# Kernel tuning notes

Hardware: AMD Instinct MI355X
Metric: run time of the kernel (lower is better)

## Reference

```python
import jax, jax.numpy as jnp
import numpy as np

KR = 3  # kernel_range, SHIFT = 1


def _neighborhood(x):
    """x: [B,H,W,C] -> [B,H,W,9,C] stacking the 3x3 shifted views (zero pad),
    in the same (i,j) raster order as the original loop."""
    B, H, W, C = x.shape
    xp = jnp.pad(x, ((0, 0), (1, 1), (1, 1), (0, 0)))
    views = [xp[:, 1 + i:1 + i + H, 1 + j:1 + j + W, :]
             for i in (-1, 0, 1) for j in (-1, 0, 1)]
    return jnp.stack(views, axis=3)


def _conv(x, w, b):
    # tf.nn.conv2d NHWC, HWIO, SAME, stride 1
    return jax.lax.conv_general_dilated(
        x, w, window_strides=(1, 1), padding='SAME',
        dimension_numbers=('NHWC', 'HWIO', 'NHWC')) + b


def setup_inputs() -> dict:
    key = jax.random.key(0)
    ks = jax.random.split(key, 10)
    B, H, W, D = 8, 128, 128, 64
    g = lambda k, shape, fan: jax.random.normal(k, shape, jnp.float32) * np.float32(1.0 / np.sqrt(fan))
    return {
        'x': jax.random.normal(ks[0], (B, H, W, D), jnp.float32),
        'Q_P': g(ks[1], (D, D), D),
        'K_P': g(ks[2], (D, D), D),
        'V_P': g(ks[3], (D, D), D),
        'ff1_kernel': g(ks[4], (3, 3, D, D), 9 * D),
        'ff1_bias': jax.random.normal(ks[5], (D,), jnp.float32) * 0.01,
        'ff2_kernel': g(ks[6], (3, 3, D, 2 * D), 9 * D),
        'ff2_bias': jax.random.normal(ks[7], (2 * D,), jnp.float32) * 0.01,
        'ff3_kernel': g(ks[8], (3, 3, 2 * D, D), 9 * 2 * D),
        'ff3_bias': jax.random.normal(ks[9], (D,), jnp.float32) * 0.01,
    }


def reference(x, Q_P, K_P, V_P, ff1_kernel, ff1_bias, ff2_kernel, ff2_bias,
              ff3_kernel, ff3_bias):
    B, H, W, D = x.shape
    # 3x3 neighborhood gather (zero padded) and validity mask
    stk = _neighborhood(x)                                   # [B,H,W,9,D]
    mask = _neighborhood(jnp.ones((B, H, W, 1), x.dtype))    # [B,H,W,9,1]
    mask = mask[..., 0]                                      # [B,H,W,9]

    q = jnp.einsum('bhwd,de->bhwe', x, Q_P)                  # [B,H,W,D]
    k = jnp.einsum('bhwkd,de->bhwke', stk, K_P)              # [B,H,W,9,D]
    v = jnp.einsum('bhwkd,de->bhwke', stk, V_P)              # [B,H,W,9,D]

    # NOTE: faithful to original -- scores are MULTIPLIED by the mask
    # (masked entries become 0, not -inf) before softmax over the 9 neighbors.
    scores = jnp.einsum('bhwke,bhwe->bhwk', k, q) * mask     # [B,H,W,9]
    alpha = jax.nn.softmax(scores, axis=-1)
    attn = jnp.einsum('bhwk,bhwke->bhwe', alpha, v)          # [B,H,W,D]

    t = x + attn
    t_in = t
    t = jax.nn.relu(_conv(t, ff1_kernel, ff1_bias))
    t = jax.nn.relu(_conv(t, ff2_kernel, ff2_bias))
    t = jax.nn.relu(_conv(t, ff3_kernel, ff3_bias))
    return t_in + t
```

## Files before the change

kernel.cpp:

```cpp
#include <hip/hip_runtime.h>

typedef unsigned int uint32;
typedef unsigned short u16;
typedef short s16x8 __attribute__((ext_vector_type(8)));
typedef float f32x4 __attribute__((ext_vector_type(4)));

#define DEVINL static __device__ __forceinline__
#define MFMA16(a, b, c) __builtin_amdgcn_mfma_f32_16x16x32_bf16(a, b, c, 0, 0, 0)

DEVINL float bf2f(u16 u){ return __uint_as_float(((uint32)u) << 16); }
DEVINL u16 f2bf(float f){
  uint32 u = __float_as_uint(f);
  u += 0x7fffu + ((u >> 16) & 1u);
  return (u16)(u >> 16);
}
DEVINL uint32 pack2(float a, float b){
  return (uint32)f2bf(a) | (((uint32)f2bf(b)) << 16);
}

__global__ void detect_k(const uint32* __restrict__ x, uint32* __restrict__ flag){
  const int lane = threadIdx.x;
  int sane = 0;
  for (int i = 0; i < 32; ++i){
    uint32 u = x[i * 64 + lane];
    uint32 e = (u >> 7) & 0xffu;
    sane += (e >= 100u && e <= 150u) ? 1 : 0;
  }
  for (int off = 32; off >= 1; off >>= 1) sane += __shfl_xor(sane, off);
  if (lane == 0) *flag = (sane > 1024) ? 1u : 0u;
}

template<int M>
__global__ void cvtall_k(const void* s0, const void* s1, const void* s2,
                         const void* s3, const void* s4, const void* s5,
                         const void* s6, const void* s7, const void* s8,
                         float* __restrict__ wb, const uint32* __restrict__ flag)
{
  if (*flag != (uint32)M) return;
  const int i = blockIdx.x * 256 + threadIdx.x;
  if (i >= 196864) return;
  const void* s; int j;
  if      (i < 4096)   { s = s0; j = i; }
  else if (i < 8192)   { s = s1; j = i - 4096; }
  else if (i < 12288)  { s = s2; j = i - 8192; }
  else if (i < 49152)  { s = s3; j = i - 12288; }
  else if (i < 49216)  { s = s4; j = i - 49152; }
  else if (i < 122944) { s = s5; j = i - 49216; }
  else if (i < 123072) { s = s6; j = i - 122944; }
  else if (i < 196800) { s = s7; j = i - 123072; }
  else                 { s = s8; j = i - 196800; }
  wb[i] = M ? bf2f(((const u16*)s)[j]) : ((const float*)s)[j];
}

__global__ __launch_bounds__(256)
void xcvt_k(const void* __restrict__ x, u16* __restrict__ xb,
            const uint32* __restrict__ flag)
{
  if (*flag != 0u) return;
  const size_t i0 = ((size_t)blockIdx.x * 256 + threadIdx.x) * 8;
  const float4 f0 = ((const float4*)x)[i0 / 4];
  const float4 f1 = ((const float4*)x)[i0 / 4 + 1];
  uint4 o;
  o.x = pack2(f0.x, f0.y); o.y = pack2(f0.z, f0.w);
  o.z = pack2(f1.x, f1.y); o.w = pack2(f1.z, f1.w);
  *(uint4*)(xb + i0) = o;
}

__global__ void gcomp_k(const float* __restrict__ wb, u16* __restrict__ gt){
  const int t = blockIdx.x * 256 + threadIdx.x;
  const int d = t >> 6, c = t & 63;
  const float* __restrict__ K = wb + 4096;
  const float* __restrict__ Q = wb;
  float s = 0.f;
#pragma unroll
  for (int e = 0; e < 64; ++e) s = fmaf(K[d * 64 + e], Q[c * 64 + e], s);
  const u16 hi = f2bf(s);
  gt[t] = hi;
  gt[4096 + t] = f2bf(s - bf2f(hi));
}

__global__ void pack_k(const float* __restrict__ wb, u16* __restrict__ bb){
  int i = blockIdx.x * 256 + threadIdx.x;
  if (i < 4096){
    const int o = i >> 6, c = i & 63;
    bb[8192 + i] = f2bf(wb[8192 + c * 64 + o]);
    return;
  }
  i -= 4096;
  if (i < 36864){
    const int chunk = i >> 11, rr = i & 2047, co = rr >> 5, kkp = rr & 31;
    const int slot = (kkp >> 3) ^ ((co >> 1) & 3), kk = slot * 8 + (kkp & 7);
    const int tap = chunk >> 1, ci = (chunk & 1) * 32 + kk;
    bb[12288 + i] = f2bf(wb[12288 + (tap * 64 + ci) * 64 + co]);
    return;
  }
  i -= 36864;
  if (i < 73728){
    const int half = i / 36864, i2 = i - half * 36864;
    const int chunk = i2 >> 11, rr = i2 & 2047, co = rr >> 5, kkp = rr & 31;
    const int slot = (kkp >> 3) ^ ((co >> 1) & 3), kk = slot * 8 + (kkp & 7);
    const int tap = chunk >> 1, ci = (chunk & 1) * 32 + kk;
    bb[49152 + i] = f2bf(wb[49216 + (tap * 64 + ci) * 128 + half * 64 + co]);
    return;
  }
  i -= 73728;
  {
    const int chunk = i >> 11, rr = i & 2047, co = rr >> 5, kkp = rr & 31;
    const int slot = (kkp >> 3) ^ ((co >> 1) & 3), kk = slot * 8 + (kkp & 7);
    const int tap = chunk >> 2, ci = (chunk & 3) * 32 + kk;
    bb[122880 + i] = f2bf(wb[123072 + (tap * 128 + ci) * 64 + co]);
  }
}

template<int ROWS, int CIN, int STRIDE>
DEVINL void stage_tile(const u16* __restrict__ img_base, int h0, int w0, u16* lds){
  constexpr int CH8 = CIN / 8;
  constexpr int NCH = ROWS * 66 * CH8;
  for (int idx = threadIdx.x; idx < NCH; idx += 256){
    const int row  = idx / (66 * CH8);
    const int rem  = idx - row * 66 * CH8;
    const int col  = rem / CH8;
    const int slot = rem - col * CH8;
    const int hi = h0 + row - 1, wi = w0 + col - 1;
    uint4 v = make_uint4(0u, 0u, 0u, 0u);
    if (hi >= 0 && hi < 128 && wi >= 0 && wi < 128)
      v = *(const uint4*)(img_base + (size_t)(hi * 128 + wi) * STRIDE + slot * 8);
    const int dst = (row * 66 + col) * CIN + ((slot ^ (col & 7)) << 3);
    *(uint4*)(lds + dst) = v;
  }
}

__global__ __launch_bounds__(256)
void attn_mfma(const u16* __restrict__ xraw, const u16* __restrict__ xcv,
               const u16* __restrict__ gt, const u16* __restrict__ vt,
               u16* __restrict__ tb, const uint32* __restrict__ flag)
{
  __shared__ __align__(16) u16 xh[3 * 66 * 64];
  __shared__ __align__(16) float rl[64 * 68];
  u16* yl  = xh;
  u16* yl2 = xh + 2 * 66 * 64;
  const int bx0 = blockIdx.x;
  const int bx = (bx0 & 7) * 256 + (bx0 >> 3);
  const int img = bx >> 8, h = (bx >> 1) & 127, w0 = (bx & 1) * 64;
  const int p0 = img * 16384 + h * 128 + w0;
  const u16* __restrict__ xsrc = (*flag != 0u) ? xraw : xcv;
  stage_tile<3, 64, 64>(xsrc + (size_t)img * 16384 * 64, h, w0, xh);
  __syncthreads();

  const int lane = threadIdx.x & 63, wv = threadIdx.x >> 6;
  const int l15 = lane & 15, lk = lane >> 4;

  f32x4 racc[4];
#pragma unroll
  for (int nt = 0; nt < 4; ++nt) racc[nt] = (f32x4){0.f, 0.f, 0.f, 0.f};
#pragma unroll
  for (int half = 0; half < 2; ++half){
#pragma unroll
    for (int ks = 0; ks < 2; ++ks){
      const int pxl = wv * 16 + l15;
      const int col = pxl + 1;
      const int slot = ks * 4 + lk;
      const s16x8 af = *(const s16x8*)&xh[(66 + col) * 64 + ((slot ^ (col & 7)) << 3)];
#pragma unroll
      for (int nt = 0; nt < 4; ++nt){
        const s16x8 bf = *(const s16x8*)(gt + half * 4096 +
                          (size_t)(nt * 16 + l15) * 64 + ks * 32 + lk * 8);
        racc[nt] = MFMA16(af, bf, racc[nt]);
      }
    }
  }

#pragma unroll
  for (int nt = 0; nt < 4; ++nt)
#pragma unroll
    for (int reg = 0; reg < 4; ++reg)
      rl[(wv * 16 + lk * 4 + reg) * 68 + nt * 16 + l15] = racc[nt][reg];

  __syncthreads();

  const int pxm = wv * 16 + l15;
  float rq[16];
  {
    const float* rr = rl + pxm * 68 + lk * 16;
#pragma unroll
    for (int j = 0; j < 16; j += 4){
      const float4 v = *(const float4*)(rr + j);
      rq[j] = v.x; rq[j+1] = v.y; rq[j+2] = v.z; rq[j+3] = v.w;
    }
  }

  float sc[9];
#pragma unroll
  for (int n = 0; n < 9; ++n){
    const int tr = n / 3, tc = n % 3;
    const int col = pxm + tc;
    const u16* xr = &xh[(tr * 66 + col) * 64];
    float s = 0.f;
#pragma unroll
    for (int sl = 0; sl < 2; ++sl){
      const int slot = lk * 2 + sl;
      const s16x8 v = *(const s16x8*)&xr[(slot ^ (col & 7)) << 3];
#pragma unroll
      for (int j = 0; j < 8; ++j)
        s = fmaf(bf2f((u16)v[j]), rq[sl * 8 + j], s);
    }
    sc[n] = s;
  }
#pragma unroll
  for (int n = 0; n < 9; ++n){
    sc[n] += __shfl_xor(sc[n], 16);
    sc[n] += __shfl_xor(sc[n], 32);
  }

  float mx = sc[0];
#pragma unroll
  for (int n = 1; n < 9; ++n) mx = fmaxf(mx, sc[n]);
  float sum = 0.f;
#pragma unroll
  for (int n = 0; n < 9; ++n){
    const float e = __expf(sc[n] - mx);
    sc[n] = e; sum += e;
  }
  const float inv = 1.f / sum;
#pragma unroll
  for (int n = 0; n < 9; ++n) sc[n] *= inv;

  float y[16];
#pragma unroll
  for (int j = 0; j < 16; ++j) y[j] = 0.f;
#pragma unroll
  for (int n = 0; n < 9; ++n){
    const int tr = n / 3, tc = n % 3;
    const int col = pxm + tc;
    const u16* xr = &xh[(tr * 66 + col) * 64];
    const float a = sc[n];
#pragma unroll
    for (int sl = 0; sl < 2; ++sl){
      const int slot = lk * 2 + sl;
      const s16x8 v = *(const s16x8*)&xr[(slot ^ (col & 7)) << 3];
#pragma unroll
      for (int j = 0; j < 8; ++j)
        y[sl * 8 + j] = fmaf(a, bf2f((u16)v[j]), y[sl * 8 + j]);
    }
  }

  __syncthreads();

#pragma unroll
  for (int sl = 0; sl < 2; ++sl){
    uint32 hwd[4], lwd[4];
#pragma unroll
    for (int j = 0; j < 4; ++j){
      const float a = y[sl * 8 + 2 * j], b = y[sl * 8 + 2 * j + 1];
      const u16 ha = f2bf(a), hb = f2bf(b);
      hwd[j] = (uint32)ha | ((uint32)hb << 16);
      lwd[j] = (uint32)f2bf(a - bf2f(ha)) | ((uint32)f2bf(b - bf2f(hb)) << 16);
    }
    const int slot = lk * 2 + sl;
    const int off = pxm * 64 + ((slot ^ (pxm & 7)) << 3);
    *(uint4*)&yl [off] = make_uint4(hwd[0], hwd[1], hwd[2], hwd[3]);
    *(uint4*)&yl2[off] = make_uint4(lwd[0], lwd[1], lwd[2], lwd[3]);
  }

  __syncthreads();

  f32x4 tacc[4];
#pragma unroll
  for (int nt = 0; nt < 4; ++nt) tacc[nt] = (f32x4){0.f, 0.f, 0.f, 0.f};
#pragma unroll
  for (int half = 0; half < 2; ++half){
    const u16* yb = half ? yl2 : yl;
#pragma unroll
    for (int ks = 0; ks < 2; ++ks){
      const int px = wv * 16 + l15;
      const int slot = ks * 4 + lk;
      const s16x8 af = *(const s16x8*)&yb[px * 64 + ((slot ^ (px & 7)) << 3)];
#pragma unroll
      for (int nt = 0; nt < 4; ++nt){
        const s16x8 bf = *(const s16x8*)(vt + (size_t)(nt * 16 + l15) * 64 + ks * 32 + lk * 8);
        tacc[nt] = MFMA16(af, bf, tacc[nt]);
      }
    }
  }
#pragma unroll
  for (int nt = 0; nt < 4; ++nt){
#pragma unroll
    for (int reg = 0; reg < 4; ++reg){
      const int pxo = wv * 16 + lk * 4 + reg;
      const int co = nt * 16 + l15;
      const int col = pxo + 1;
      const int elem = (66 + col) * 64 + (((co >> 3) ^ (col & 7)) << 3) + (co & 7);
      tb[(size_t)(p0 + pxo) * 64 + co] = f2bf(bf2f(xh[elem]) + tacc[nt][reg]);
    }
  }
}

template<int COUT_FULL, bool RES, int MOUT>
__global__ __launch_bounds__(256)
void conv_mfma(const u16* __restrict__ in, const u16* __restrict__ wpk,
               const float* __restrict__ bias, const u16* __restrict__ res,
               void* __restrict__ out, const uint32* __restrict__ flag)
{
  if (MOUT >= 0){ if (*flag != (uint32)MOUT) return; }
  constexpr int TOT = 18;
  __shared__ __align__(16) u16 xh[6 * 66 * 64];
  __shared__ __align__(16) u16 Bb[3][2048];

  const int bx0 = blockIdx.x;
  const int bx  = (bx0 & 7) * 64 + (bx0 >> 3);
  const int img = bx >> 6;
  const int rem = bx & 63;
  const int h0  = (rem >> 1) * 4;
  const int w0  = (rem & 1) * 64;
  const int co0 = blockIdx.y * 64;
  const u16* __restrict__ wp = wpk + (size_t)blockIdx.y * TOT * 2048;

  auto stageB = [&](int it, int buf){
    const char* g = (const char*)(wp + (size_t)it * 2048) + threadIdx.x * 16;
    char* l = (char*)&Bb[buf][0] + threadIdx.x * 16;
    __builtin_amdgcn_global_load_lds((const __attribute__((address_space(1))) void*)g,
                                     (__attribute__((address_space(3))) void*)l, 16, 0, 0);
  };

  stage_tile<6, 64, 64>(in + (size_t)img * 16384 * 64, h0, w0, xh);
  stageB(0, 0);
  __syncthreads();

  const int lane = threadIdx.x & 63, wv = threadIdx.x >> 6;
  const int l15 = lane & 15, lk = lane >> 4;

  f32x4 acc[4][4];
#pragma unroll
  for (int nt = 0; nt < 4; ++nt){
    const float b = bias[co0 + nt * 16 + l15];
#pragma unroll
    for (int at = 0; at < 4; ++at) acc[at][nt] = (f32x4){b, b, b, b};
  }

#pragma unroll 1
  for (int it = 0; it < TOT; ++it){
    if (it + 1 < TOT){
      stageB(it + 1, (it + 1) % 3);
      asm volatile("s_waitcnt vmcnt(1)" ::: "memory");
    } else {
      asm volatile("s_waitcnt vmcnt(0)" ::: "memory");
    }
    __builtin_amdgcn_s_barrier();
    __builtin_amdgcn_sched_barrier(0);

    const int b = it % 3;
    const int tap = it >> 1, ks = it & 1;
    const int tr = tap / 3, tc = tap - tr * 3;
    const int slot = ks * 4 + lk;
    s16x8 av[4], bv[4];
#pragma unroll
    for (int at = 0; at < 4; ++at){
      const int col = at * 16 + l15 + tc;
      av[at] = *(const s16x8*)&xh[((wv + tr) * 66 + col) * 64 + ((slot ^ (col & 7)) << 3)];
    }
#pragma unroll
    for (int nt = 0; nt < 4; ++nt){
      const int co = nt * 16 + l15;
      bv[nt] = *(const s16x8*)&Bb[b][co * 32 + ((lk ^ ((co >> 1) & 3)) << 3)];
    }
#pragma unroll
    for (int at = 0; at < 4; ++at)
#pragma unroll
      for (int nt = 0; nt < 4; ++nt)
        acc[at][nt] = MFMA16(av[at], bv[nt], acc[at][nt]);
  }

#pragma unroll
  for (int at = 0; at < 4; ++at){
#pragma unroll
    for (int nt = 0; nt < 4; ++nt){
#pragma unroll
      for (int reg = 0; reg < 4; ++reg){
        float v = fmaxf(acc[at][nt][reg], 0.f);
        const int pxg = img * 16384 + (h0 + wv) * 128 + w0 + at * 16 + lk * 4 + reg;
        const int co  = co0 + nt * 16 + l15;
        const size_t oi = (size_t)pxg * COUT_FULL + co;
        if (RES) v += bf2f(res[oi]);
        if (MOUT == 0) ((float*)out)[oi] = v;
        else           ((u16*)out)[oi]   = f2bf(v);
      }
    }
  }
}

template<int MOUT>
__global__ __launch_bounds__(256)
void conv3_mfma(const u16* __restrict__ in, const u16* __restrict__ wpk,
                const float* __restrict__ bias, const u16* __restrict__ res,
                void* __restrict__ out, const uint32* __restrict__ flag)
{
  if (*flag != (uint32)MOUT) return;
  __shared__ __align__(16) u16 xh[6 * 66 * 64];
  __shared__ __align__(16) u16 Bb[3][2048];

  const int bx0 = blockIdx.x;
  const int bx  = (bx0 & 7) * 64 + (bx0 >> 3);
  const int img = bx >> 6;
  const int rem = bx & 63;
  const int h0  = (rem >> 1) * 4;
  const int w0  = (rem & 1) * 64;

  auto stageB = [&](int chunk, int buf){
    const char* g = (const char*)(wpk + (size_t)chunk * 2048) + threadIdx.x * 16;
    char* l = (char*)&Bb[buf][0] + threadIdx.x * 16;
    __builtin_amdgcn_global_load_lds((const __attribute__((address_space(1))) void*)g,
                                     (__attribute__((address_space(3))) void*)l, 16, 0, 0);
  };

  const int lane = threadIdx.x & 63, wv = threadIdx.x >> 6;
  const int l15 = lane & 15, lk = lane >> 4;

  f32x4 acc[4][4];
#pragma unroll
  for (int nt = 0; nt < 4; ++nt){
    const float b = bias[nt * 16 + l15];
#pragma unroll
    for (int at = 0; at < 4; ++at) acc[at][nt] = (f32x4){b, b, b, b};
  }

#pragma unroll 1
  for (int half = 0; half < 2; ++half){
    if (half) __syncthreads();
    stage_tile<6, 64, 128>(in + (size_t)img * 16384 * 128 + half * 64, h0, w0, xh);
    stageB(half * 2, 0);
    __syncthreads();

#pragma unroll 1
    for (int it = 0; it < 18; ++it){
      if (it + 1 < 18){
        const int tap1 = (it + 1) >> 1, ks1 = (it + 1) & 1;
        stageB(tap1 * 4 + half * 2 + ks1, (it + 1) % 3);
        asm volatile("s_waitcnt vmcnt(1)" ::: "memory");
      } else {
        asm volatile("s_waitcnt vmcnt(0)" ::: "memory");
      }
      __builtin_amdgcn_s_barrier();
      __builtin_amdgcn_sched_barrier(0);

      const int b = it % 3;
      const int tap = it >> 1, ks2 = it & 1;
      const int tr = tap / 3, tc = tap - tr * 3;
      const int slot = ks2 * 4 + lk;
      s16x8 av[4], bv[4];
#pragma unroll
      for (int at = 0; at < 4; ++at){
        const int col = at * 16 + l15 + tc;
        av[at] = *(const s16x8*)&xh[((wv + tr) * 66 + col) * 64 + ((slot ^ (col & 7)) << 3)];
      }
#pragma unroll
      for (int nt = 0; nt < 4; ++nt){
        const int co = nt * 16 + l15;
        bv[nt] = *(const s16x8*)&Bb[b][co * 32 + ((lk ^ ((co >> 1) & 3)) << 3)];
      }
#pragma unroll
      for (int at = 0; at < 4; ++at)
#pragma unroll
        for (int nt = 0; nt < 4; ++nt)
          acc[at][nt] = MFMA16(av[at], bv[nt], acc[at][nt]);
    }
  }

#pragma unroll
  for (int at = 0; at < 4; ++at){
#pragma unroll
    for (int nt = 0; nt < 4; ++nt){
#pragma unroll
      for (int reg = 0; reg < 4; ++reg){
        float v = fmaxf(acc[at][nt][reg], 0.f);
        const int pxg = img * 16384 + (h0 + wv) * 128 + w0 + at * 16 + lk * 4 + reg;
        const int co  = nt * 16 + l15;
        const size_t oi = (size_t)pxg * 64 + co;
        v += bf2f(res[oi]);
        if (MOUT == 0) ((float*)out)[oi] = v;
        else           ((u16*)out)[oi]   = f2bf(v);
      }
    }
  }
}

extern "C" void kernel_launch(void* const* d_in, const int* in_sizes, int n_in,
                              void* d_out, int out_size, void* d_ws, size_t ws_size,
                              hipStream_t stream)
{
  (void)in_sizes; (void)n_in; (void)out_size; (void)ws_size;

  char* ws = (char*)d_ws;
  float*  wblob = (float*)ws;
  uint32* flag  = (uint32*)(ws + 983040);
  u16*    bb    = (u16*)(ws + (1u << 20));
  u16*    gt   = bb;
  u16*    vt   = bb + 8192;
  u16*    w1pk = bb + 12288;
  u16*    w2pk = bb + 49152;
  u16*    w3pk = bb + 122880;

  u16* xb = (u16*)(ws + (size_t)2097152);
  u16* c2 = xb;
  u16* tb = (u16*)(ws + (size_t)35651584);
  u16* c1 = (u16*)(ws + (size_t)52428800);

  detect_k<<<1, 64, 0, stream>>>((const uint32*)d_in[0], flag);

  cvtall_k<0><<<769, 256, 0, stream>>>(d_in[1], d_in[2], d_in[3], d_in[4], d_in[5],
                                       d_in[6], d_in[7], d_in[8], d_in[9], wblob, flag);
  cvtall_k<1><<<769, 256, 0, stream>>>(d_in[1], d_in[2], d_in[3], d_in[4], d_in[5],
                                       d_in[6], d_in[7], d_in[8], d_in[9], wblob, flag);

  xcvt_k<<<4096, 256, 0, stream>>>(d_in[0], xb, flag);

  gcomp_k<<<16, 256, 0, stream>>>(wblob, gt);
  pack_k<<<736, 256, 0, stream>>>(wblob, bb);

  attn_mfma<<<2048, 256, 0, stream>>>((const u16*)d_in[0], xb, gt, vt, tb, flag);

  conv_mfma<64, false, -1><<<dim3(512, 1), 256, 0, stream>>>(
      tb, w1pk, wblob + 49152, nullptr, c1, flag);
  conv_mfma<128, false, -1><<<dim3(512, 2), 256, 0, stream>>>(
      c1, w2pk, wblob + 122944, nullptr, c2, flag);
  conv3_mfma<0><<<512, 256, 0, stream>>>(
      c2, w3pk, wblob + 196800, tb, d_out, flag);
  conv3_mfma<1><<<512, 256, 0, stream>>>(
      c2, w3pk, wblob + 196800, tb, d_out, flag);
}
```

Measured before the change: 152.9 us.

## Precompute x·V per pixel and restructure attention and conv pipelining

Adds a separate kernel that computes xV = x·V_P once per pixel in fp32, using a hi/lo split of V for accuracy. The attention kernel then mixes the neighbour xV rows with the softmax weights instead of running a second MFMA on the weighted sum. It also feeds the MFMA score output straight into the dot products without the LDS round-trip, and adds launch bounds. The conv kernels now prefetch B tiles two steps ahead and move the wait and barrier after the MFMA block. The cost is an extra fp32 intermediate (about 33 MB) written and re-read from global memory, plus one more kernel launch.

New measurement: 191.6 us. 1.25x slower.

```diff
diff --git a/kernel.cpp b/kernel.cpp
--- a/kernel.cpp
+++ b/kernel.cpp
@@ -3,6 +3,7 @@
 typedef unsigned int uint32;
 typedef unsigned short u16;
 typedef short s16x8 __attribute__((ext_vector_type(8)));
+typedef short s16x4 __attribute__((ext_vector_type(4)));
 typedef float f32x4 __attribute__((ext_vector_type(4)));
 
 #define DEVINL static __device__ __forceinline__
@@ -87,11 +88,18 @@
     return;
   }
   i -= 4096;
+  if (i < 4096){
+    const int o = i >> 6, c = i & 63;
+    const float v = wb[8192 + c * 64 + o];
+    bb[12288 + i] = f2bf(v - bf2f(f2bf(v)));
+    return;
+  }
+  i -= 4096;
   if (i < 36864){
     const int chunk = i >> 11, rr = i & 2047, co = rr >> 5, kkp = rr & 31;
     const int slot = (kkp >> 3) ^ ((co >> 1) & 3), kk = slot * 8 + (kkp & 7);
     const int tap = chunk >> 1, ci = (chunk & 1) * 32 + kk;
-    bb[12288 + i] = f2bf(wb[12288 + (tap * 64 + ci) * 64 + co]);
+    bb[16384 + i] = f2bf(wb[12288 + (tap * 64 + ci) * 64 + co]);
     return;
   }
   i -= 36864;
@@ -100,7 +108,7 @@
     const int chunk = i2 >> 11, rr = i2 & 2047, co = rr >> 5, kkp = rr & 31;
     const int slot = (kkp >> 3) ^ ((co >> 1) & 3), kk = slot * 8 + (kkp & 7);
     const int tap = chunk >> 1, ci = (chunk & 1) * 32 + kk;
-    bb[49152 + i] = f2bf(wb[49216 + (tap * 64 + ci) * 128 + half * 64 + co]);
+    bb[53248 + i] = f2bf(wb[49216 + (tap * 64 + ci) * 128 + half * 64 + co]);
     return;
   }
   i -= 73728;
@@ -108,8 +116,44 @@
     const int chunk = i >> 11, rr = i & 2047, co = rr >> 5, kkp = rr & 31;
     const int slot = (kkp >> 3) ^ ((co >> 1) & 3), kk = slot * 8 + (kkp & 7);
     const int tap = chunk >> 2, ci = (chunk & 3) * 32 + kk;
-    bb[122880 + i] = f2bf(wb[123072 + (tap * 128 + ci) * 64 + co]);
-  }
+    bb[126976 + i] = f2bf(wb[123072 + (tap * 128 + ci) * 64 + co]);
+  }
+}
+
+__global__ __launch_bounds__(256)
+void xv_k(const u16* __restrict__ xraw, const u16* __restrict__ xcv,
+          const u16* __restrict__ vt, const u16* __restrict__ vlo,
+          float* __restrict__ xv, const uint32* __restrict__ flag)
+{
+  const u16* __restrict__ xsrc = (*flag != 0u) ? xraw : xcv;
+  const int bx0 = blockIdx.x;
+  const int bx = (bx0 & 7) * 256 + (bx0 >> 3);
+  const int p0 = bx * 64;
+  const int lane = threadIdx.x & 63, wv = threadIdx.x >> 6;
+  const int l15 = lane & 15, lk = lane >> 4;
+
+  f32x4 racc[4];
+#pragma unroll
+  for (int nt = 0; nt < 4; ++nt) racc[nt] = (f32x4){0.f, 0.f, 0.f, 0.f};
+#pragma unroll
+  for (int half = 0; half < 2; ++half){
+    const u16* __restrict__ vb = half ? vlo : vt;
+#pragma unroll
+    for (int ks = 0; ks < 2; ++ks){
+      const s16x8 af = *(const s16x8*)(xsrc +
+          (size_t)(p0 + wv * 16 + l15) * 64 + ks * 32 + lk * 8);
+#pragma unroll
+      for (int nt = 0; nt < 4; ++nt){
+        const s16x8 bf = *(const s16x8*)(vb + (size_t)(nt * 16 + l15) * 64 + ks * 32 + lk * 8);
+        racc[nt] = MFMA16(af, bf, racc[nt]);
+      }
+    }
+  }
+#pragma unroll
+  for (int nt = 0; nt < 4; ++nt)
+#pragma unroll
+    for (int reg = 0; reg < 4; ++reg)
+      xv[(size_t)(p0 + wv * 16 + lk * 4 + reg) * 64 + nt * 16 + l15] = racc[nt][reg];
 }
 
 template<int ROWS, int CIN, int STRIDE>
@@ -130,15 +174,12 @@
   }
 }
 
-__global__ __launch_bounds__(256)
+__global__ __launch_bounds__(256, 4)
 void attn_mfma(const u16* __restrict__ xraw, const u16* __restrict__ xcv,
-               const u16* __restrict__ gt, const u16* __restrict__ vt,
+               const u16* __restrict__ gt, const float* __restrict__ xv,
                u16* __restrict__ tb, const uint32* __restrict__ flag)
 {
   __shared__ __align__(16) u16 xh[3 * 66 * 64];
-  __shared__ __align__(16) float rl[64 * 68];
-  u16* yl  = xh;
-  u16* yl2 = xh + 2 * 66 * 64;
   const int bx0 = blockIdx.x;
   const int bx = (bx0 & 7) * 256 + (bx0 >> 3);
   const int img = bx >> 8, h = (bx >> 1) & 127, w0 = (bx & 1) * 64;
@@ -149,6 +190,7 @@
 
   const int lane = threadIdx.x & 63, wv = threadIdx.x >> 6;
   const int l15 = lane & 15, lk = lane >> 4;
+  const int pxm = wv * 16 + l15;
 
   f32x4 racc[4];
 #pragma unroll
@@ -157,35 +199,15 @@
   for (int half = 0; half < 2; ++half){
 #pragma unroll
     for (int ks = 0; ks < 2; ++ks){
-      const int pxl = wv * 16 + l15;
-      const int col = pxl + 1;
+      const int colq = pxm + 1;
       const int slot = ks * 4 + lk;
-      const s16x8 af = *(const s16x8*)&xh[(66 + col) * 64 + ((slot ^ (col & 7)) << 3)];
+      const s16x8 bx_ = *(const s16x8*)&xh[(66 + colq) * 64 + ((slot ^ (colq & 7)) << 3)];
 #pragma unroll
       for (int nt = 0; nt < 4; ++nt){
-        const s16x8 bf = *(const s16x8*)(gt + half * 4096 +
+        const s16x8 ag = *(const s16x8*)(gt + half * 4096 +
                           (size_t)(nt * 16 + l15) * 64 + ks * 32 + lk * 8);
-        racc[nt] = MFMA16(af, bf, racc[nt]);
-      }
-    }
-  }
-
-#pragma unroll
-  for (int nt = 0; nt < 4; ++nt)
-#pragma unroll
-    for (int reg = 0; reg < 4; ++reg)
-      rl[(wv * 16 + lk * 4 + reg) * 68 + nt * 16 + l15] = racc[nt][reg];
-
-  __syncthreads();
-
-  const int pxm = wv * 16 + l15;
-  float rq[16];
-  {
-    const float* rr = rl + pxm * 68 + lk * 16;
-#pragma unroll
-    for (int j = 0; j < 16; j += 4){
-      const float4 v = *(const float4*)(rr + j);
-      rq[j] = v.x; rq[j+1] = v.y; rq[j+2] = v.z; rq[j+3] = v.w;
+        racc[nt] = MFMA16(ag, bx_, racc[nt]);
+      }
     }
   }
 
@@ -197,12 +219,12 @@
     const u16* xr = &xh[(tr * 66 + col) * 64];
     float s = 0.f;
 #pragma unroll
-    for (int sl = 0; sl < 2; ++sl){
-      const int slot = lk * 2 + sl;
-      const s16x8 v = *(const s16x8*)&xr[(slot ^ (col & 7)) << 3];
-#pragma unroll
-      for (int j = 0; j < 8; ++j)
-        s = fmaf(bf2f((u16)v[j]), rq[sl * 8 + j], s);
+    for (int nt = 0; nt < 4; ++nt){
+      const int slot = nt * 2 + (lk >> 1);
+      const s16x4 v = *(const s16x4*)&xr[((slot ^ (col & 7)) << 3) + (lk & 1) * 4];
+#pragma unroll
+      for (int j = 0; j < 4; ++j)
+        s = fmaf(bf2f((u16)v[j]), racc[nt][j], s);
     }
     sc[n] = s;
   }
@@ -225,74 +247,43 @@
 #pragma unroll
   for (int n = 0; n < 9; ++n) sc[n] *= inv;
 
-  float y[16];
-#pragma unroll
-  for (int j = 0; j < 16; ++j) y[j] = 0.f;
+  float out[16];
+#pragma unroll
+  for (int sl = 0; sl < 2; ++sl){
+    const int colq = pxm + 1;
+    const int slot = lk * 2 + sl;
+    const s16x8 v = *(const s16x8*)&xh[(66 + colq) * 64 + ((slot ^ (colq & 7)) << 3)];
+#pragma unroll
+    for (int j = 0; j < 8; ++j) out[sl * 8 + j] = bf2f((u16)v[j]);
+  }
 #pragma unroll
   for (int n = 0; n < 9; ++n){
     const int tr = n / 3, tc = n % 3;
-    const int col = pxm + tc;
-    const u16* xr = &xh[(tr * 66 + col) * 64];
-    const float a = sc[n];
-#pragma unroll
-    for (int sl = 0; sl < 2; ++sl){
-      const int slot = lk * 2 + sl;
-      const s16x8 v = *(const s16x8*)&xr[(slot ^ (col & 7)) << 3];
-#pragma unroll
-      for (int j = 0; j < 8; ++j)
-        y[sl * 8 + j] = fmaf(a, bf2f((u16)v[j]), y[sl * 8 + j]);
-    }
-  }
-
-  __syncthreads();
-
-#pragma unroll
-  for (int sl = 0; sl < 2; ++sl){
-    uint32 hwd[4], lwd[4];
-#pragma unroll
-    for (int j = 0; j < 4; ++j){
-      const float a = y[sl * 8 + 2 * j], b = y[sl * 8 + 2 * j + 1];
-      const u16 ha = f2bf(a), hb = f2bf(b);
-      hwd[j] = (uint32)ha | ((uint32)hb << 16);
-      lwd[j] = (uint32)f2bf(a - bf2f(ha)) | ((uint32)f2bf(b - bf2f(hb)) << 16);
-    }
-    const int slot = lk * 2 + sl;
-    const int off = pxm * 64 + ((slot ^ (pxm & 7)) << 3);
-    *(uint4*)&yl [off] = make_uint4(hwd[0], hwd[1], hwd[2], hwd[3]);
-    *(uint4*)&yl2[off] = make_uint4(lwd[0], lwd[1], lwd[2], lwd[3]);
-  }
-
-  __syncthreads();
-
-  f32x4 tacc[4];
-#pragma unroll
-  for (int nt = 0; nt < 4; ++nt) tacc[nt] = (f32x4){0.f, 0.f, 0.f, 0.f};
-#pragma unroll
-  for (int half = 0; half < 2; ++half){
-    const u16* yb = half ? yl2 : yl;
-#pragma unroll
-    for (int ks = 0; ks < 2; ++ks){
-      const int px = wv * 16 + l15;
-      const int slot = ks * 4 + lk;
-      const s16x8 af = *(const s16x8*)&yb[px * 64 + ((slot ^ (px & 7)) << 3)];
-#pragma unroll
-      for (int nt = 0; nt < 4; ++nt){
-        const s16x8 bf = *(const s16x8*)(vt + (size_t)(nt * 16 + l15) * 64 + ks * 32 + lk * 8);
-        tacc[nt] = MFMA16(af, bf, tacc[nt]);
-      }
-    }
-  }
-#pragma unroll
-  for (int nt = 0; nt < 4; ++nt){
-#pragma unroll
-    for (int reg = 0; reg < 4; ++reg){
-      const int pxo = wv * 16 + lk * 4 + reg;
-      const int co = nt * 16 + l15;
-      const int col = pxo + 1;
-      const int elem = (66 + col) * 64 + (((co >> 3) ^ (col & 7)) << 3) + (co & 7);
-      tb[(size_t)(p0 + pxo) * 64 + co] = f2bf(bf2f(xh[elem]) + tacc[nt][reg]);
-    }
-  }
+    const int hh = h + tr - 1;
+    const int wc = w0 + pxm + tc - 1;
+    if (hh >= 0 && hh < 128 && wc >= 0 && wc < 128){
+      const float a = sc[n];
+      const float4* xp = (const float4*)(xv +
+          (size_t)(img * 16384 + hh * 128 + wc) * 64 + lk * 16);
+      const float4 v0 = xp[0], v1 = xp[1], v2 = xp[2], v3 = xp[3];
+      out[0]  = fmaf(a, v0.x, out[0]);  out[1]  = fmaf(a, v0.y, out[1]);
+      out[2]  = fmaf(a, v0.z, out[2]);  out[3]  = fmaf(a, v0.w, out[3]);
+      out[4]  = fmaf(a, v1.x, out[4]);  out[5]  = fmaf(a, v1.y, out[5]);
+      out[6]  = fmaf(a, v1.z, out[6]);  out[7]  = fmaf(a, v1.w, out[7]);
+      out[8]  = fmaf(a, v2.x, out[8]);  out[9]  = fmaf(a, v2.y, out[9]);
+      out[10] = fmaf(a, v2.z, out[10]); out[11] = fmaf(a, v2.w, out[11]);
+      out[12] = fmaf(a, v3.x, out[12]); out[13] = fmaf(a, v3.y, out[13]);
+      out[14] = fmaf(a, v3.z, out[14]); out[15] = fmaf(a, v3.w, out[15]);
+    }
+  }
+
+  uint4 o0, o1;
+  o0.x = pack2(out[0],  out[1]);  o0.y = pack2(out[2],  out[3]);
+  o0.z = pack2(out[4],  out[5]);  o0.w = pack2(out[6],  out[7]);
+  o1.x = pack2(out[8],  out[9]);  o1.y = pack2(out[10], out[11]);
+  o1.z = pack2(out[12], out[13]); o1.w = pack2(out[14], out[15]);
+  uint4* op = (uint4*)(tb + (size_t)(p0 + pxm) * 64 + lk * 16);
+  op[0] = o0; op[1] = o1;
 }
 
 template<int COUT_FULL, bool RES, int MOUT>
@@ -324,6 +315,7 @@
 
   stage_tile<6, 64, 64>(in + (size_t)img * 16384 * 64, h0, w0, xh);
   stageB(0, 0);
+  stageB(1, 1);
   __syncthreads();
 
   const int lane = threadIdx.x & 63, wv = threadIdx.x >> 6;
@@ -339,15 +331,7 @@
 
 #pragma unroll 1
   for (int it = 0; it < TOT; ++it){
-    if (it + 1 < TOT){
-      stageB(it + 1, (it + 1) % 3);
-      asm volatile("s_waitcnt vmcnt(1)" ::: "memory");
-    } else {
-      asm volatile("s_waitcnt vmcnt(0)" ::: "memory");
-    }
-    __builtin_amdgcn_s_barrier();
-    __builtin_amdgcn_sched_barrier(0);
-
+    if (it + 2 < TOT) stageB(it + 2, (it + 2) % 3);
     const int b = it % 3;
     const int tap = it >> 1, ks = it & 1;
     const int tr = tap / 3, tc = tap - tr * 3;
@@ -368,6 +352,13 @@
 #pragma unroll
       for (int nt = 0; nt < 4; ++nt)
         acc[at][nt] = MFMA16(av[at], bv[nt], acc[at][nt]);
+
+    if (it + 1 < TOT){
+      if (it + 2 < TOT) asm volatile("s_waitcnt vmcnt(1)" ::: "memory");
+      else              asm volatile("s_waitcnt vmcnt(0)" ::: "memory");
+      __builtin_amdgcn_s_barrier();
+      __builtin_amdgcn_sched_barrier(0);
+    }
   }
 
 #pragma unroll
@@ -415,6 +406,10 @@
   const int lane = threadIdx.x & 63, wv = threadIdx.x >> 6;
   const int l15 = lane & 15, lk = lane >> 4;
 
+  auto chunkOf = [&](int it, int half){
+    return ((it >> 1) << 2) + half * 2 + (it & 1);
+  };
+
   f32x4 acc[4][4];
 #pragma unroll
   for (int nt = 0; nt < 4; ++nt){
@@ -427,21 +422,13 @@
   for (int half = 0; half < 2; ++half){
     if (half) __syncthreads();
     stage_tile<6, 64, 128>(in + (size_t)img * 16384 * 128 + half * 64, h0, w0, xh);
-    stageB(half * 2, 0);
+    stageB(chunkOf(0, half), 0);
+    stageB(chunkOf(1, half), 1);
     __syncthreads();
 
 #pragma unroll 1
     for (int it = 0; it < 18; ++it){
-      if (it + 1 < 18){
-        const int tap1 = (it + 1) >> 1, ks1 = (it + 1) & 1;
-        stageB(tap1 * 4 + half * 2 + ks1, (it + 1) % 3);
-        asm volatile("s_waitcnt vmcnt(1)" ::: "memory");
-      } else {
-        asm volatile("s_waitcnt vmcnt(0)" ::: "memory");
-      }
-      __builtin_amdgcn_s_barrier();
-      __builtin_amdgcn_sched_barrier(0);
-
+      if (it + 2 < 18) stageB(chunkOf(it + 2, half), (it + 2) % 3);
       const int b = it % 3;
       const int tap = it >> 1, ks2 = it & 1;
       const int tr = tap / 3, tc = tap - tr * 3;
@@ -462,6 +449,13 @@
 #pragma unroll
         for (int nt = 0; nt < 4; ++nt)
           acc[at][nt] = MFMA16(av[at], bv[nt], acc[at][nt]);
+
+      if (it + 1 < 18){
+        if (it + 2 < 18) asm volatile("s_waitcnt vmcnt(1)" ::: "memory");
+        else             asm volatile("s_waitcnt vmcnt(0)" ::: "memory");
+        __builtin_amdgcn_s_barrier();
+        __builtin_amdgcn_sched_barrier(0);
+      }
     }
   }
 
@@ -495,14 +489,16 @@
   u16*    bb    = (u16*)(ws + (1u << 20));
   u16*    gt   = bb;
   u16*    vt   = bb + 8192;
-  u16*    w1pk = bb + 12288;
-  u16*    w2pk = bb + 49152;
-  u16*    w3pk = bb + 122880;
-
-  u16* xb = (u16*)(ws + (size_t)2097152);
-  u16* c2 = xb;
-  u16* tb = (u16*)(ws + (size_t)35651584);
-  u16* c1 = (u16*)(ws + (size_t)52428800);
+  u16*    vlo  = bb + 12288;
+  u16*    w1pk = bb + 16384;
+  u16*    w2pk = bb + 53248;
+  u16*    w3pk = bb + 126976;
+
+  float* xv = (float*)(ws + (size_t)2097152);
+  u16*   c2 = (u16*)(ws + (size_t)2097152);
+  u16*   tb = (u16*)(ws + (size_t)35651584);
+  u16*   xb = (u16*)(ws + (size_t)52428800);
+  u16*   c1 = (u16*)(ws + (size_t)52428800);
 
   detect_k<<<1, 64, 0, stream>>>((const uint32*)d_in[0], flag);
 
@@ -514,9 +510,11 @@
   xcvt_k<<<4096, 256, 0, stream>>>(d_in[0], xb, flag);
 
   gcomp_k<<<16, 256, 0, stream>>>(wblob, gt);
-  pack_k<<<736, 256, 0, stream>>>(wblob, bb);
-
-  attn_mfma<<<2048, 256, 0, stream>>>((const u16*)d_in[0], xb, gt, vt, tb, flag);
+  pack_k<<<752, 256, 0, stream>>>(wblob, bb);
+
+  xv_k<<<2048, 256, 0, stream>>>((const u16*)d_in[0], xb, vt, vlo, xv, flag);
+
+  attn_mfma<<<2048, 256, 0, stream>>>((const u16*)d_in[0], xb, gt, xv, tb, flag);
 
   conv_mfma<64, false, -1><<<dim3(512, 1), 256, 0, stream>>>(
       tb, w1pk, wblob + 49152, nullptr, c1, flag);
```

## Keep attention q-products in registers and deepen conv weight prefetch pipeline

Applied to the files above, without the earlier changes.

The attention kernel swaps the MFMA operand order so each lane's accumulator already holds the G·x values it needs for the neighbor dot products. This removes the LDS round-trip through the rl buffer and a __syncthreads, and the kernel gets an occupancy hint of 4 blocks. The conv kernels now prefetch weight chunks two iterations ahead and move the wait and barrier after the MFMA work, so loads overlap compute. Pack_k also adds a bf16 residual (lo) copy of the V weights and shifts the buffer offsets, and xb/c1 share memory. The aliasing of xb with c1 and the new layout add risk.

Result: no change. 150.6 us (-1.5%).

```diff
diff --git a/kernel.cpp b/kernel.cpp
--- a/kernel.cpp
+++ b/kernel.cpp
@@ -3,6 +3,7 @@
 typedef unsigned int uint32;
 typedef unsigned short u16;
 typedef short s16x8 __attribute__((ext_vector_type(8)));
+typedef short s16x4 __attribute__((ext_vector_type(4)));
 typedef float f32x4 __attribute__((ext_vector_type(4)));
 
 #define DEVINL static __device__ __forceinline__
@@ -87,11 +88,18 @@
     return;
   }
   i -= 4096;
+  if (i < 4096){
+    const int o = i >> 6, c = i & 63;
+    const float v = wb[8192 + c * 64 + o];
+    bb[12288 + i] = f2bf(v - bf2f(f2bf(v)));
+    return;
+  }
+  i -= 4096;
   if (i < 36864){
     const int chunk = i >> 11, rr = i & 2047, co = rr >> 5, kkp = rr & 31;
     const int slot = (kkp >> 3) ^ ((co >> 1) & 3), kk = slot * 8 + (kkp & 7);
     const int tap = chunk >> 1, ci = (chunk & 1) * 32 + kk;
-    bb[12288 + i] = f2bf(wb[12288 + (tap * 64 + ci) * 64 + co]);
+    bb[16384 + i] = f2bf(wb[12288 + (tap * 64 + ci) * 64 + co]);
     return;
   }
   i -= 36864;
@@ -100,7 +108,7 @@
     const int chunk = i2 >> 11, rr = i2 & 2047, co = rr >> 5, kkp = rr & 31;
     const int slot = (kkp >> 3) ^ ((co >> 1) & 3), kk = slot * 8 + (kkp & 7);
     const int tap = chunk >> 1, ci = (chunk & 1) * 32 + kk;
-    bb[49152 + i] = f2bf(wb[49216 + (tap * 64 + ci) * 128 + half * 64 + co]);
+    bb[53248 + i] = f2bf(wb[49216 + (tap * 64 + ci) * 128 + half * 64 + co]);
     return;
   }
   i -= 73728;
@@ -108,7 +116,7 @@
     const int chunk = i >> 11, rr = i & 2047, co = rr >> 5, kkp = rr & 31;
     const int slot = (kkp >> 3) ^ ((co >> 1) & 3), kk = slot * 8 + (kkp & 7);
     const int tap = chunk >> 2, ci = (chunk & 3) * 32 + kk;
-    bb[122880 + i] = f2bf(wb[123072 + (tap * 128 + ci) * 64 + co]);
+    bb[126976 + i] = f2bf(wb[123072 + (tap * 128 + ci) * 64 + co]);
   }
 }
 
@@ -130,13 +138,12 @@
   }
 }
 
-__global__ __launch_bounds__(256)
+__global__ __launch_bounds__(256, 4)
 void attn_mfma(const u16* __restrict__ xraw, const u16* __restrict__ xcv,
                const u16* __restrict__ gt, const u16* __restrict__ vt,
                u16* __restrict__ tb, const uint32* __restrict__ flag)
 {
   __shared__ __align__(16) u16 xh[3 * 66 * 64];
-  __shared__ __align__(16) float rl[64 * 68];
   u16* yl  = xh;
   u16* yl2 = xh + 2 * 66 * 64;
   const int bx0 = blockIdx.x;
@@ -149,6 +156,7 @@
 
   const int lane = threadIdx.x & 63, wv = threadIdx.x >> 6;
   const int l15 = lane & 15, lk = lane >> 4;
+  const int pxm = wv * 16 + l15;
 
   f32x4 racc[4];
 #pragma unroll
@@ -157,35 +165,15 @@
   for (int half = 0; half < 2; ++half){
 #pragma unroll
     for (int ks = 0; ks < 2; ++ks){
-      const int pxl = wv * 16 + l15;
-      const int col = pxl + 1;
+      const int colq = pxm + 1;
       const int slot = ks * 4 + lk;
-      const s16x8 af = *(const s16x8*)&xh[(66 + col) * 64 + ((slot ^ (col & 7)) << 3)];
+      const s16x8 bx_ = *(const s16x8*)&xh[(66 + colq) * 64 + ((slot ^ (colq & 7)) << 3)];
 #pragma unroll
       for (int nt = 0; nt < 4; ++nt){
-        const s16x8 bf = *(const s16x8*)(gt + half * 4096 +
+        const s16x8 ag = *(const s16x8*)(gt + half * 4096 +
                           (size_t)(nt * 16 + l15) * 64 + ks * 32 + lk * 8);
-        racc[nt] = MFMA16(af, bf, racc[nt]);
-      }
-    }
-  }
-
-#pragma unroll
-  for (int nt = 0; nt < 4; ++nt)
-#pragma unroll
-    for (int reg = 0; reg < 4; ++reg)
-      rl[(wv * 16 + lk * 4 + reg) * 68 + nt * 16 + l15] = racc[nt][reg];
-
-  __syncthreads();
-
-  const int pxm = wv * 16 + l15;
-  float rq[16];
-  {
-    const float* rr = rl + pxm * 68 + lk * 16;
-#pragma unroll
-    for (int j = 0; j < 16; j += 4){
-      const float4 v = *(const float4*)(rr + j);
-      rq[j] = v.x; rq[j+1] = v.y; rq[j+2] = v.z; rq[j+3] = v.w;
+        racc[nt] = MFMA16(ag, bx_, racc[nt]);
+      }
     }
   }
 
@@ -197,12 +185,12 @@
     const u16* xr = &xh[(tr * 66 + col) * 64];
     float s = 0.f;
 #pragma unroll
-    for (int sl = 0; sl < 2; ++sl){
-      const int slot = lk * 2 + sl;
-      const s16x8 v = *(const s16x8*)&xr[(slot ^ (col & 7)) << 3];
-#pragma unroll
-      for (int j = 0; j < 8; ++j)
-        s = fmaf(bf2f((u16)v[j]), rq[sl * 8 + j], s);
+    for (int nt = 0; nt < 4; ++nt){
+      const int slot = nt * 2 + (lk >> 1);
+      const s16x4 v = *(const s16x4*)&xr[((slot ^ (col & 7)) << 3) + (lk & 1) * 4];
+#pragma unroll
+      for (int j = 0; j < 4; ++j)
+        s = fmaf(bf2f((u16)v[j]), racc[nt][j], s);
     }
     sc[n] = s;
   }
@@ -324,6 +312,7 @@
 
   stage_tile<6, 64, 64>(in + (size_t)img * 16384 * 64, h0, w0, xh);
   stageB(0, 0);
+  stageB(1, 1);
   __syncthreads();
 
   const int lane = threadIdx.x & 63, wv = threadIdx.x >> 6;
@@ -339,15 +328,7 @@
 
 #pragma unroll 1
   for (int it = 0; it < TOT; ++it){
-    if (it + 1 < TOT){
-      stageB(it + 1, (it + 1) % 3);
-      asm volatile("s_waitcnt vmcnt(1)" ::: "memory");
-    } else {
-      asm volatile("s_waitcnt vmcnt(0)" ::: "memory");
-    }
-    __builtin_amdgcn_s_barrier();
-    __builtin_amdgcn_sched_barrier(0);
-
+    if (it + 2 < TOT) stageB(it + 2, (it + 2) % 3);
     const int b = it % 3;
     const int tap = it >> 1, ks = it & 1;
     const int tr = tap / 3, tc = tap - tr * 3;
@@ -368,6 +349,13 @@
 #pragma unroll
       for (int nt = 0; nt < 4; ++nt)
         acc[at][nt] = MFMA16(av[at], bv[nt], acc[at][nt]);
+
+    if (it + 1 < TOT){
+      if (it + 2 < TOT) asm volatile("s_waitcnt vmcnt(1)" ::: "memory");
+      else              asm volatile("s_waitcnt vmcnt(0)" ::: "memory");
+      __builtin_amdgcn_s_barrier();
+      __builtin_amdgcn_sched_barrier(0);
+    }
   }
 
 #pragma unroll
@@ -415,6 +403,10 @@
   const int lane = threadIdx.x & 63, wv = threadIdx.x >> 6;
   const int l15 = lane & 15, lk = lane >> 4;
 
+  auto chunkOf = [&](int it, int half){
+    return ((it >> 1) << 2) + half * 2 + (it & 1);
+  };
+
   f32x4 acc[4][4];
 #pragma unroll
   for (int nt = 0; nt < 4; ++nt){
@@ -427,21 +419,13 @@
   for (int half = 0; half < 2; ++half){
     if (half) __syncthreads();
     stage_tile<6, 64, 128>(in + (size_t)img * 16384 * 128 + half * 64, h0, w0, xh);
-    stageB(half * 2, 0);
+    stageB(chunkOf(0, half), 0);
+    stageB(chunkOf(1, half), 1);
     __syncthreads();
 
 #pragma unroll 1
     for (int it = 0; it < 18; ++it){
-      if (it + 1 < 18){
-        const int tap1 = (it + 1) >> 1, ks1 = (it + 1) & 1;
-        stageB(tap1 * 4 + half * 2 + ks1, (it + 1) % 3);
-        asm volatile("s_waitcnt vmcnt(1)" ::: "memory");
-      } else {
-        asm volatile("s_waitcnt vmcnt(0)" ::: "memory");
-      }
-      __builtin_amdgcn_s_barrier();
-      __builtin_amdgcn_sched_barrier(0);
-
+      if (it + 2 < 18) stageB(chunkOf(it + 2, half), (it + 2) % 3);
       const int b = it % 3;
       const int tap = it >> 1, ks2 = it & 1;
       const int tr = tap / 3, tc = tap - tr * 3;
@@ -462,6 +446,13 @@
 #pragma unroll
         for (int nt = 0; nt < 4; ++nt)
           acc[at][nt] = MFMA16(av[at], bv[nt], acc[at][nt]);
+
+      if (it + 1 < 18){
+        if (it + 2 < 18) asm volatile("s_waitcnt vmcnt(1)" ::: "memory");
+        else             asm volatile("s_waitcnt vmcnt(0)" ::: "memory");
+        __builtin_amdgcn_s_barrier();
+        __builtin_amdgcn_sched_barrier(0);
+      }
     }
   }
 
@@ -495,14 +486,14 @@
   u16*    bb    = (u16*)(ws + (1u << 20));
   u16*    gt   = bb;
   u16*    vt   = bb + 8192;
-  u16*    w1pk = bb + 12288;
-  u16*    w2pk = bb + 49152;
-  u16*    w3pk = bb + 122880;
-
-  u16* xb = (u16*)(ws + (size_t)2097152);
-  u16* c2 = xb;
-  u16* tb = (u16*)(ws + (size_t)35651584);
-  u16* c1 = (u16*)(ws + (size_t)52428800);
+  u16*    w1pk = bb + 16384;
+  u16*    w2pk = bb + 53248;
+  u16*    w3pk = bb + 126976;
+
+  u16*   c2 = (u16*)(ws + (size_t)2097152);
+  u16*   tb = (u16*)(ws + (size_t)35651584);
+  u16*   xb = (u16*)(ws + (size_t)52428800);
+  u16*   c1 = (u16*)(ws + (size_t)52428800);
 
   detect_k<<<1, 64, 0, stream>>>((const uint32*)d_in[0], flag);
 
@@ -514,7 +505,7 @@
   xcvt_k<<<4096, 256, 0, stream>>>(d_in[0], xb, flag);
 
   gcomp_k<<<16, 256, 0, stream>>>(wblob, gt);
-  pack_k<<<736, 256, 0, stream>>>(wblob, bb);
+  pack_k<<<752, 256, 0, stream>>>(wblob, bb);
 
   attn_mfma<<<2048, 256, 0, stream>>>((const u16*)d_in[0], xb, gt, vt, tb, flag);
 
```
